# Kernel tuning notes

Hardware: AMD Instinct MI355X
Metric: run time of the kernel (lower is better)

Reference implementation:

```python
import jax, jax.numpy as jnp
import numpy as np

NEG_INF = -1.0e9
VALID_THRESH = -1.0e8
EPS = 1e-12


def _l2_normalize(x):
    n = jnp.linalg.norm(x, axis=-1, keepdims=True)
    return x / jnp.maximum(n, EPS)


def setup_inputs() -> dict:
    key = jax.random.key(0)
    k1, k2, k3, k4 = jax.random.split(key, 4)
    B, Nq, Nd, D = 64, 32, 256, 128
    return {
        "query_embeds": jax.random.normal(k1, (B, Nq, D), dtype=jnp.float32),
        "query_mask": jax.random.randint(k2, (B, Nq), 0, 2, dtype=jnp.int32),
        "doc_embeds": jax.random.normal(k3, (B, Nd, D), dtype=jnp.float32),
        "doc_mask": jax.random.randint(k4, (B, Nd), 0, 2, dtype=jnp.int32),
    }


def reference(query_embeds, query_mask, doc_embeds, doc_mask):
    # normalize=True, symmetric=True path
    q = _l2_normalize(query_embeds)
    d = _l2_normalize(doc_embeds)
    qm = query_mask.astype(jnp.float32)[..., None]  # [B, Nq, 1]
    dm = doc_mask.astype(jnp.float32)[..., None]    # [B, Nd, 1]
    q = q * qm
    d = d * dm

    # token_sims: [Bq, Bd, Nq, Nd]
    token_sims = jnp.einsum("qtd,csd->qcts", q, d)
    # pair mask: [Bq,1,Nq,1] * [1,Bd,1,Nd]
    mask = qm[:, None, :, :] * dm[None, :, :, 0][:, :, None, :].transpose(1, 0, 2, 3)
    masked_sims = jnp.where(mask > 0, token_sims, NEG_INF)

    # query -> doc max over doc tokens
    q2d = jnp.max(masked_sims, axis=-1)          # [Bq, Bd, Nq]
    valid_q = (q2d > VALID_THRESH).astype(jnp.float32)
    q2d = jnp.where(valid_q > 0, q2d, 0.0)
    cnt_q = jnp.maximum(jnp.sum(valid_q, axis=-1), 1.0)
    q2d_score = jnp.sum(q2d, axis=-1) / cnt_q    # [Bq, Bd]

    # doc -> query max over query tokens
    d2q = jnp.max(masked_sims, axis=-2)          # [Bq, Bd, Nd]
    valid_d = (d2q > VALID_THRESH).astype(jnp.float32)
    d2q = jnp.where(valid_d > 0, d2q, 0.0)
    cnt_d = jnp.maximum(jnp.sum(valid_d, axis=-1), 1.0)
    d2q_score = jnp.sum(d2q, axis=-1) / cnt_d    # [Bq, Bd]

    return (q2d_score + d2q_score) / 2.0
```

## Files before the change

kernel.cpp:

```cpp
#include <hip/hip_runtime.h>
#include <hip/hip_bf16.h>
#include <stdint.h>

typedef short bf16x8 __attribute__((ext_vector_type(8)));
typedef short short8 __attribute__((ext_vector_type(8)));
typedef float f32x4 __attribute__((ext_vector_type(4)));

#define B_   64
#define NQ   32
#define ND   256
#define DIM  128
#define MT   4
#define NEG_INF_F (-1.0e9f)
#define VALID_F   (-1.0e8f)

__global__ __launch_bounds__(512, 2) void chamfer_one(
    const float* __restrict__ q,
    const int* __restrict__ qmask,
    const float* __restrict__ d,
    const int* __restrict__ dmask,
    float* __restrict__ out)
{
    __shared__ __hip_bfloat16 ldsD[ND * DIM];
    __shared__ __hip_bfloat16 ldsQ[4 * NQ * DIM];
    __shared__ float s_cmax[MT][ND];
    __shared__ float s_rmaxT[MT][NQ][8];

    const int bd  = blockIdx.x & 63;
    const int g   = blockIdx.x >> 6;
    const int tid = threadIdx.x;
    const int w   = tid >> 6;
    const int l   = tid & 63;
    const int lr  = l & 15;
    const int lk  = l >> 4;
    const int grp = tid >> 4;
    const int sub = tid & 15;

    const float* Dsrc = d + (size_t)bd * ND * DIM;

    float4 dva[8], dvb[8];
    int    dmk[8];
    #pragma unroll
    for (int it = 0; it < 8; ++it) {
        const int row = it * 32 + grp;
        dva[it] = *reinterpret_cast<const float4*>(Dsrc + row * DIM + sub * 8);
        dvb[it] = *reinterpret_cast<const float4*>(Dsrc + row * DIM + sub * 8 + 4);
        dmk[it] = dmask[bd * ND + row];
    }

    float4 qva[4], qvb[4];
    int    qmk[4];
    {
        const float* Qsrc = q + (size_t)(g * 16) * NQ * DIM;
        #pragma unroll
        for (int it = 0; it < 4; ++it) {
            const int row = it * 32 + grp;
            qva[it] = *reinterpret_cast<const float4*>(Qsrc + row * DIM + sub * 8);
            qvb[it] = *reinterpret_cast<const float4*>(Qsrc + row * DIM + sub * 8 + 4);
            qmk[it] = qmask[(g * 16) * NQ + row];
        }
    }

    #pragma unroll
    for (int it = 0; it < 8; ++it) {
        const int row = it * 32 + grp;
        const float4 v0 = dva[it], v1 = dvb[it];
        float ss = v0.x*v0.x + v0.y*v0.y + v0.z*v0.z + v0.w*v0.w
                 + v1.x*v1.x + v1.y*v1.y + v1.z*v1.z + v1.w*v1.w;
        #pragma unroll
        for (int off = 1; off <= 8; off <<= 1) ss += __shfl_xor(ss, off);
        const float scale = dmk[it] ? (1.0f / fmaxf(sqrtf(ss), 1e-12f)) : 0.0f;
        short8 o;
        const float f[8] = {v0.x, v0.y, v0.z, v0.w, v1.x, v1.y, v1.z, v1.w};
        #pragma unroll
        for (int j = 0; j < 8; ++j) {
            __hip_bfloat16 b = __float2bfloat16(f[j] * scale);
            o[j] = *reinterpret_cast<short*>(&b);
        }
        *reinterpret_cast<short8*>((char*)&ldsD[0] + row * 256 + ((sub ^ (row & 7)) << 4)) = o;
    }

    #pragma unroll 1
    for (int mm = 0; mm < 4; ++mm) {
        const int bq0 = g * 16 + mm * MT;

        if (mm > 0) {
            const float* Qsrc = q + (size_t)bq0 * NQ * DIM;
            #pragma unroll
            for (int it = 0; it < 4; ++it) {
                const int row = it * 32 + grp;
                qva[it] = *reinterpret_cast<const float4*>(Qsrc + row * DIM + sub * 8);
                qvb[it] = *reinterpret_cast<const float4*>(Qsrc + row * DIM + sub * 8 + 4);
                qmk[it] = qmask[bq0 * NQ + row];
            }
        }

        #pragma unroll
        for (int it = 0; it < 4; ++it) {
            const int row = it * 32 + grp;
            const float4 v0 = qva[it], v1 = qvb[it];
            float ss = v0.x*v0.x + v0.y*v0.y + v0.z*v0.z + v0.w*v0.w
                     + v1.x*v1.x + v1.y*v1.y + v1.z*v1.z + v1.w*v1.w;
            #pragma unroll
            for (int off = 1; off <= 8; off <<= 1) ss += __shfl_xor(ss, off);
            const float scale = qmk[it] ? (1.0f / fmaxf(sqrtf(ss), 1e-12f)) : 0.0f;
            short8 o;
            const float f[8] = {v0.x, v0.y, v0.z, v0.w, v1.x, v1.y, v1.z, v1.w};
            #pragma unroll
            for (int j = 0; j < 8; ++j) {
                __hip_bfloat16 b = __float2bfloat16(f[j] * scale);
                o[j] = *reinterpret_cast<short*>(&b);
            }
            *reinterpret_cast<short8*>((char*)&ldsQ[0] + row * 256 + ((sub ^ (row & 7)) << 4)) = o;
        }

        float qneg[MT][2][4];
        float dneg[MT][2];
        #pragma unroll
        for (int m = 0; m < MT; ++m) {
            #pragma unroll
            for (int mi = 0; mi < 2; ++mi) {
                const int4 qi = *reinterpret_cast<const int4*>(&qmask[(bq0 + m) * NQ + mi * 16 + lk * 4]);
                qneg[m][mi][0] = qi.x ? 0.0f : NEG_INF_F;
                qneg[m][mi][1] = qi.y ? 0.0f : NEG_INF_F;
                qneg[m][mi][2] = qi.z ? 0.0f : NEG_INF_F;
                qneg[m][mi][3] = qi.w ? 0.0f : NEG_INF_F;
            }
            #pragma unroll
            for (int ni = 0; ni < 2; ++ni)
                dneg[m][ni] = dmask[(bq0 + m) * ND + w * 32 + ni * 16 + lr] ? 0.0f : NEG_INF_F;
        }

        __syncthreads();

        f32x4 acc[MT][2][2] = {};
        #pragma unroll
        for (int kk = 0; kk < 4; ++kk) {
            const int cL = kk * 4 + lk;
            bf16x8 bfr[2];
            #pragma unroll
            for (int ni = 0; ni < 2; ++ni) {
                const int rowd = w * 32 + ni * 16 + lr;
                bfr[ni] = *reinterpret_cast<const bf16x8*>(
                    (const char*)&ldsD[0] + rowd * 256 + ((cL ^ (rowd & 7)) << 4));
            }
            #pragma unroll
            for (int m = 0; m < MT; ++m) {
                #pragma unroll
                for (int mi = 0; mi < 2; ++mi) {
                    const int rowq = m * NQ + mi * 16 + lr;
                    const bf16x8 a = *reinterpret_cast<const bf16x8*>(
                        (const char*)&ldsQ[0] + rowq * 256 + ((cL ^ (rowq & 7)) << 4));
                    #pragma unroll
                    for (int ni = 0; ni < 2; ++ni)
                        acc[m][mi][ni] = __builtin_amdgcn_mfma_f32_16x16x32_bf16(a, bfr[ni], acc[m][mi][ni], 0, 0, 0);
                }
            }
        }

        #pragma unroll
        for (int m = 0; m < MT; ++m) {
            float rmax[2][4];
            float cmax[2] = {NEG_INF_F, NEG_INF_F};
            #pragma unroll
            for (int mi = 0; mi < 2; ++mi) {
                #pragma unroll
                for (int r = 0; r < 4; ++r) {
                    const float t0 = acc[m][mi][0][r] + (qneg[m][mi][r] + dneg[m][0]);
                    const float t1 = acc[m][mi][1][r] + (qneg[m][mi][r] + dneg[m][1]);
                    rmax[mi][r] = fmaxf(t0, t1);
                    cmax[0] = fmaxf(cmax[0], t0);
                    cmax[1] = fmaxf(cmax[1], t1);
                }
            }
            #pragma unroll
            for (int ni = 0; ni < 2; ++ni) {
                cmax[ni] = fmaxf(cmax[ni], __shfl_xor(cmax[ni], 16));
                cmax[ni] = fmaxf(cmax[ni], __shfl_xor(cmax[ni], 32));
            }
            if (lk == 0) {
                #pragma unroll
                for (int ni = 0; ni < 2; ++ni)
                    s_cmax[m][w * 32 + ni * 16 + lr] = cmax[ni];
            }
            #pragma unroll
            for (int mi = 0; mi < 2; ++mi)
                #pragma unroll
                for (int r = 0; r < 4; ++r) {
                    #pragma unroll
                    for (int off = 1; off <= 8; off <<= 1)
                        rmax[mi][r] = fmaxf(rmax[mi][r], __shfl_xor(rmax[mi][r], off));
                }
            if (lr == 0) {
                #pragma unroll
                for (int mi = 0; mi < 2; ++mi)
                    #pragma unroll
                    for (int r = 0; r < 4; ++r)
                        s_rmaxT[m][mi * 16 + lk * 4 + r][w] = rmax[mi][r];
            }
        }
        __syncthreads();

        if (w < MT) {
            const int m = w;
            const float4 cm = *reinterpret_cast<const float4*>(&s_cmax[m][l * 4]);
            float sd = 0.0f, cd = 0.0f;
            if (cm.x > VALID_F) { sd += cm.x; cd += 1.0f; }
            if (cm.y > VALID_F) { sd += cm.y; cd += 1.0f; }
            if (cm.z > VALID_F) { sd += cm.z; cd += 1.0f; }
            if (cm.w > VALID_F) { sd += cm.w; cd += 1.0f; }
            float sq = 0.0f, cq = 0.0f;
            if (l < NQ) {
                const float4 a = *reinterpret_cast<const float4*>(&s_rmaxT[m][l][0]);
                const float4 b = *reinterpret_cast<const float4*>(&s_rmaxT[m][l][4]);
                const float v = fmaxf(fmaxf(fmaxf(a.x, a.y), fmaxf(a.z, a.w)),
                                      fmaxf(fmaxf(b.x, b.y), fmaxf(b.z, b.w)));
                if (v > VALID_F) { sq = v; cq = 1.0f; }
            }
            #pragma unroll
            for (int off = 1; off <= 32; off <<= 1) {
                sd += __shfl_xor(sd, off);
                cd += __shfl_xor(cd, off);
                sq += __shfl_xor(sq, off);
                cq += __shfl_xor(cq, off);
            }
            if (l == 0) {
                const float q2d = sq / fmaxf(cq, 1.0f);
                const float d2q = sd / fmaxf(cd, 1.0f);
                out[(bq0 + m) * B_ + bd] = 0.5f * (q2d + d2q);
            }
        }
    }
}

extern "C" void kernel_launch(void* const* d_in, const int* in_sizes, int n_in,
                              void* d_out, int out_size, void* d_ws, size_t ws_size,
                              hipStream_t stream) {
    const float* q  = (const float*)d_in[0];
    const int*   qm = (const int*)d_in[1];
    const float* d  = (const float*)d_in[2];
    const int*   dm = (const int*)d_in[3];
    float* out = (float*)d_out;

    chamfer_one<<<B_ * 4, 512, 0, stream>>>(q, qm, d, dm, out);
}
```

Baseline: 97.52 us.

## Keep doc fragments in registers, halve query tile, double grid

```diff
diff --git a/kernel.cpp b/kernel.cpp
--- a/kernel.cpp
+++ b/kernel.cpp
@@ -10,19 +10,18 @@
 #define NQ   32
 #define ND   256
 #define DIM  128
-#define MT   4
+#define MT   2
 #define NEG_INF_F (-1.0e9f)
 #define VALID_F   (-1.0e8f)
 
-__global__ __launch_bounds__(512, 2) void chamfer_one(
+__global__ __launch_bounds__(512, 4) void chamfer_one(
     const float* __restrict__ q,
     const int* __restrict__ qmask,
     const float* __restrict__ d,
     const int* __restrict__ dmask,
     float* __restrict__ out)
 {
-    __shared__ __hip_bfloat16 ldsD[ND * DIM];
-    __shared__ __hip_bfloat16 ldsQ[4 * NQ * DIM];
+    __shared__ __hip_bfloat16 ldsQ[2 * NQ * DIM];
     __shared__ float s_cmax[MT][ND];
     __shared__ float s_rmaxT[MT][NQ][8];
 
@@ -38,56 +37,68 @@
 
     const float* Dsrc = d + (size_t)bd * ND * DIM;
 
-    float4 dva[8], dvb[8];
-    int    dmk[8];
+    float4 dv[2][4][2];
+    int    dmk[2];
     #pragma unroll
-    for (int it = 0; it < 8; ++it) {
-        const int row = it * 32 + grp;
-        dva[it] = *reinterpret_cast<const float4*>(Dsrc + row * DIM + sub * 8);
-        dvb[it] = *reinterpret_cast<const float4*>(Dsrc + row * DIM + sub * 8 + 4);
-        dmk[it] = dmask[bd * ND + row];
-    }
-
-    float4 qva[4], qvb[4];
-    int    qmk[4];
+    for (int ni = 0; ni < 2; ++ni) {
+        const int r = w * 32 + ni * 16 + lr;
+        #pragma unroll
+        for (int kk = 0; kk < 4; ++kk) {
+            const float* p = Dsrc + r * DIM + kk * 32 + lk * 8;
+            dv[ni][kk][0] = *reinterpret_cast<const float4*>(p);
+            dv[ni][kk][1] = *reinterpret_cast<const float4*>(p + 4);
+        }
+        dmk[ni] = dmask[bd * ND + r];
+    }
+
+    float4 qva[2], qvb[2];
+    int    qmk[2];
     {
-        const float* Qsrc = q + (size_t)(g * 16) * NQ * DIM;
-        #pragma unroll
-        for (int it = 0; it < 4; ++it) {
+        const float* Qsrc = q + (size_t)(g * 8) * NQ * DIM;
+        #pragma unroll
+        for (int it = 0; it < 2; ++it) {
             const int row = it * 32 + grp;
             qva[it] = *reinterpret_cast<const float4*>(Qsrc + row * DIM + sub * 8);
             qvb[it] = *reinterpret_cast<const float4*>(Qsrc + row * DIM + sub * 8 + 4);
-            qmk[it] = qmask[(g * 16) * NQ + row];
-        }
-    }
-
+            qmk[it] = qmask[(g * 8) * NQ + row];
+        }
+    }
+
+    bf16x8 Bfr[4][2];
     #pragma unroll
-    for (int it = 0; it < 8; ++it) {
-        const int row = it * 32 + grp;
-        const float4 v0 = dva[it], v1 = dvb[it];
-        float ss = v0.x*v0.x + v0.y*v0.y + v0.z*v0.z + v0.w*v0.w
-                 + v1.x*v1.x + v1.y*v1.y + v1.z*v1.z + v1.w*v1.w;
-        #pragma unroll
-        for (int off = 1; off <= 8; off <<= 1) ss += __shfl_xor(ss, off);
-        const float scale = dmk[it] ? (1.0f / fmaxf(sqrtf(ss), 1e-12f)) : 0.0f;
-        short8 o;
-        const float f[8] = {v0.x, v0.y, v0.z, v0.w, v1.x, v1.y, v1.z, v1.w};
-        #pragma unroll
-        for (int j = 0; j < 8; ++j) {
-            __hip_bfloat16 b = __float2bfloat16(f[j] * scale);
-            o[j] = *reinterpret_cast<short*>(&b);
-        }
-        *reinterpret_cast<short8*>((char*)&ldsD[0] + row * 256 + ((sub ^ (row & 7)) << 4)) = o;
+    for (int ni = 0; ni < 2; ++ni) {
+        float ss = 0.0f;
+        #pragma unroll
+        for (int kk = 0; kk < 4; ++kk) {
+            const float4 a = dv[ni][kk][0], b = dv[ni][kk][1];
+            ss += a.x*a.x + a.y*a.y + a.z*a.z + a.w*a.w
+                + b.x*b.x + b.y*b.y + b.z*b.z + b.w*b.w;
+        }
+        ss += __shfl_xor(ss, 16);
+        ss += __shfl_xor(ss, 32);
+        const float scale = dmk[ni] ? (1.0f / fmaxf(sqrtf(ss), 1e-12f)) : 0.0f;
+        #pragma unroll
+        for (int kk = 0; kk < 4; ++kk) {
+            const float f[8] = {dv[ni][kk][0].x, dv[ni][kk][0].y, dv[ni][kk][0].z, dv[ni][kk][0].w,
+                                dv[ni][kk][1].x, dv[ni][kk][1].y, dv[ni][kk][1].z, dv[ni][kk][1].w};
+            short8 o;
+            #pragma unroll
+            for (int j = 0; j < 8; ++j) {
+                __hip_bfloat16 h = __float2bfloat16(f[j] * scale);
+                o[j] = *reinterpret_cast<short*>(&h);
+            }
+            Bfr[kk][ni] = o;
+        }
     }
 
     #pragma unroll 1
     for (int mm = 0; mm < 4; ++mm) {
-        const int bq0 = g * 16 + mm * MT;
+        const int bq0 = g * 8 + mm * MT;
 
         if (mm > 0) {
             const float* Qsrc = q + (size_t)bq0 * NQ * DIM;
             #pragma unroll
-            for (int it = 0; it < 4; ++it) {
+            for (int it = 0; it < 2; ++it) {
                 const int row = it * 32 + grp;
                 qva[it] = *reinterpret_cast<const float4*>(Qsrc + row * DIM + sub * 8);
                 qvb[it] = *reinterpret_cast<const float4*>(Qsrc + row * DIM + sub * 8 + 4);
@@ -96,7 +107,7 @@
         }
 
         #pragma unroll
-        for (int it = 0; it < 4; ++it) {
+        for (int it = 0; it < 2; ++it) {
             const int row = it * 32 + grp;
             const float4 v0 = qva[it], v1 = qvb[it];
             float ss = v0.x*v0.x + v0.y*v0.y + v0.z*v0.z + v0.w*v0.w
@@ -137,13 +148,6 @@
         #pragma unroll
         for (int kk = 0; kk < 4; ++kk) {
             const int cL = kk * 4 + lk;
-            bf16x8 bfr[2];
-            #pragma unroll
-            for (int ni = 0; ni < 2; ++ni) {
-                const int rowd = w * 32 + ni * 16 + lr;
-                bfr[ni] = *reinterpret_cast<const bf16x8*>(
-                    (const char*)&ldsD[0] + rowd * 256 + ((cL ^ (rowd & 7)) << 4));
-            }
             #pragma unroll
             for (int m = 0; m < MT; ++m) {
                 #pragma unroll
@@ -153,7 +157,7 @@
                         (const char*)&ldsQ[0] + rowq * 256 + ((cL ^ (rowq & 7)) << 4));
                     #pragma unroll
                     for (int ni = 0; ni < 2; ++ni)
-                        acc[m][mi][ni] = __builtin_amdgcn_mfma_f32_16x16x32_bf16(a, bfr[ni], acc[m][mi][ni], 0, 0, 0);
+                        acc[m][mi][ni] = __builtin_amdgcn_mfma_f32_16x16x32_bf16(a, Bfr[kk][ni], acc[m][mi][ni], 0, 0, 0);
                 }
             }
         }
@@ -242,5 +246,5 @@
     const int*   dm = (const int*)d_in[3];
     float* out = (float*)d_out;
 
-    chamfer_one<<<B_ * 4, 512, 0, stream>>>(q, qm, d, dm, out);
+    chamfer_one<<<B_ * 8, 512, 0, stream>>>(q, qm, d, dm, out);
 }
```

Measured after the change: 105.8 us. 8.5% more time.
